# Kernel tuning notes

Hardware: AMD Instinct MI355X
Metric: run time of the kernel (lower is better)

The kernel has to match this reference:

```python
import jax, jax.numpy as jnp
import numpy as np

QMIN, QMAX = -128, 127  # get_quantized_range(8)


def setup_inputs() -> dict:
    key = jax.random.key(0)
    k1, k2, k3, k4 = jax.random.split(key, 4)
    N, IN, OUT = 8192, 4096, 4096
    x = jax.random.randint(k1, (N, IN), QMIN, QMAX + 1, dtype=jnp.int32).astype(jnp.int8)
    weight = jax.random.randint(k2, (OUT, IN), QMIN, QMAX + 1, dtype=jnp.int32).astype(jnp.int8)
    bias = jax.random.randint(k3, (OUT,), -1000, 1000, dtype=jnp.int32)
    weight_scale = jax.random.uniform(k4, (OUT,), dtype=jnp.float32, minval=1e-3, maxval=2e-2)
    return {
        "x": x,
        "weight": weight,
        "bias": bias,
        "weight_scale": weight_scale,
        "input_scale": 0.05,
        "output_scale": 0.1,
        "output_zero_point": -3,
    }


def reference(x, weight, bias, weight_scale, input_scale, output_scale, output_zero_point):
    # int8 GEMM accumulated in int32 (matches CPU path of the torch code)
    acc = jnp.matmul(x.astype(jnp.int32), weight.astype(jnp.int32).T) + bias[None, :]
    # fused per-channel dequant/requant epilogue
    scale = (input_scale * weight_scale / output_scale)[None, :]  # [1, OUT]
    out = acc.astype(jnp.float32) * scale + output_zero_point
    out = jnp.clip(jnp.round(out), QMIN, QMAX).astype(jnp.int8)
    return out
```

## Files before the change

### kernel.cpp

```cpp
#include <hip/hip_runtime.h>
#include <stdint.h>
#include <stddef.h>

typedef int v4i __attribute__((ext_vector_type(4)));

#define GLOAD16(gp, lp) __builtin_amdgcn_global_load_lds( \
    (const __attribute__((address_space(1))) void*)(gp),  \
    (__attribute__((address_space(3))) void*)(lp), 16, 0, 0)

#define PH_BAR()     __builtin_amdgcn_s_barrier()
#define WAIT_LGKM0() asm volatile("s_waitcnt lgkmcnt(0)" ::: "memory")
#define WAIT_VM(n)   asm volatile("s_waitcnt vmcnt(" #n ")" ::: "memory")
#define SCHED_FENCE() __builtin_amdgcn_sched_barrier(0)
#define PRIO1() __builtin_amdgcn_s_setprio(1)
#define PRIO0() __builtin_amdgcn_s_setprio(0)

static __device__ __forceinline__ int pack4(int a, int b, int c, int d) {
    return (a & 255) | ((b & 255) << 8) | ((c & 255) << 16) | (d << 24);
}

__global__ __launch_bounds__(256) void pack2_kernel(const int* __restrict__ srcA, v4i* __restrict__ dstA, int nA,
                                                    const int* __restrict__ srcB, v4i* __restrict__ dstB, int nB) {
    int i = blockIdx.x * blockDim.x + threadIdx.x;
    const int* src; v4i* dst;
    if (i < nA) { src = srcA; dst = dstA; }
    else { i -= nA; if (i >= nB) return; src = srcB; dst = dstB; }
    const v4i* s = reinterpret_cast<const v4i*>(src) + (size_t)i * 4;
    v4i v0 = s[0], v1 = s[1], v2 = s[2], v3 = s[3];
    v4i r;
    r.x = pack4(v0.x, v0.y, v0.z, v0.w);
    r.y = pack4(v1.x, v1.y, v1.z, v1.w);
    r.z = pack4(v2.x, v2.y, v2.z, v2.w);
    r.w = pack4(v3.x, v3.y, v3.z, v3.w);
    dst[i] = r;
}

__global__ __launch_bounds__(512, 2) void gemm_q8_8ph(
    const char* __restrict__ Apk, const char* __restrict__ Bpk,
    const int* __restrict__ bias, const float* __restrict__ wscale,
    const float* __restrict__ is_p, const float* __restrict__ os_p,
    const int* __restrict__ zp_p,
    int* __restrict__ out, int K, int Ncols)
{
    __shared__ char lds[131072];

    const int tid  = threadIdx.x;
    const int wid  = tid >> 6;
    const int lane = tid & 63;
    const int l7 = lane & 7, l3 = lane >> 3;
    const int lo16 = lane & 15, hi = lane >> 4;

    int swz;
    {
        const int nwg = gridDim.x;
        const int q = nwg >> 3, r = nwg & 7;
        const int xcd = blockIdx.x & 7;
        const int base = (xcd < r) ? xcd * (q + 1) : r * (q + 1) + (xcd - r) * q;
        swz = base + (blockIdx.x >> 3);
    }
    const int nbc  = Ncols >> 8;
    const int brow = swz / nbc, bcol = swz % nbc;

    const int wr = wid >> 2, wc = wid & 3;

    const char* Ab = Apk + (size_t)(brow * 256 + wid * 8 + l3) * K + ((l7 ^ l3) << 4);
    const char* Bb = Bpk + (size_t)(bcol * 256 + wid * 8 + l3) * K + ((l7 ^ l3) << 4);

    const int colsw0 = (hi << 4) ^ (l7 << 4);
    const int colsw1 = colsw0 ^ 64;
    const int aRow = ((wr << 7) + lo16) << 7;
    const int bRow = ((wc << 6) + lo16) << 7;

    v4i acc[8][4];
#pragma unroll
    for (int m = 0; m < 8; ++m)
#pragma unroll
        for (int n = 0; n < 4; ++n)
            acc[m][n] = (v4i){0, 0, 0, 0};

    v4i af[4][2], bf[2][2], bf2[2][2];

    auto stage = [&](const char* gb, int ldsOp, int bufo, int h, int t) {
        const char* g = gb + (size_t)(h * 128) * K + ((size_t)t << 7);
        char* l = lds + (ldsOp + bufo + (h << 14) + (wid << 10));
        GLOAD16(g, l);
        GLOAD16(g + (size_t)64 * K, l + 8192);
    };
    auto ldA = [&](int bufo, int mh) {
#pragma unroll
        for (int m = 0; m < 4; ++m) {
            const int base = bufo + aRow + (mh << 13) + (m << 11);
            af[m][0] = *(const v4i*)(lds + base + colsw0);
            af[m][1] = *(const v4i*)(lds + base + colsw1);
        }
    };
    auto ldB = [&](v4i (&bx)[2][2], int bufo, int n0) {
#pragma unroll
        for (int n = 0; n < 2; ++n) {
            const int base = 65536 + bufo + bRow + ((n0 + n) << 11);
            bx[n][0] = *(const v4i*)(lds + base + colsw0);
            bx[n][1] = *(const v4i*)(lds + base + colsw1);
        }
    };

#define MFMA_Q(mo, bfx, no) do {                                                  \
    _Pragma("unroll") for (int m_ = 0; m_ < 4; ++m_)                              \
    _Pragma("unroll") for (int n_ = 0; n_ < 2; ++n_)                              \
    _Pragma("unroll") for (int s_ = 0; s_ < 2; ++s_)                              \
        acc[(mo) + m_][(no) + n_] = __builtin_amdgcn_mfma_i32_16x16x64_i8(        \
            af[m_][s_], bfx[n_][s_], acc[(mo) + m_][(no) + n_], 0, 0, 0);         \
} while (0)

    stage(Ab, 0,     0,     0, 0);  stage(Ab, 0,     0,     1, 0);
    stage(Bb, 65536, 0,     0, 0);  stage(Bb, 65536, 0,     1, 0);
    stage(Bb, 65536, 32768, 0, 1);  stage(Bb, 65536, 32768, 1, 1);
    WAIT_VM(4);
    PH_BAR();
    ldB(bf, 0, 0);

    const int niter = K >> 8;
    for (int i = 0; i < niter - 1; ++i) {
        SCHED_FENCE();
        const int tO1 = 2 * i + 1, tE = 2 * i + 2, tO = 2 * i + 3;

        ldA(0, 0);
        stage(Ab, 0, 32768, 0, tO1);
        PH_BAR(); WAIT_LGKM0();
        PRIO1(); MFMA_Q(0, bf, 0); PRIO0();
        PH_BAR();
        ldB(bf2, 0, 2);
        stage(Ab, 0, 32768, 1, tO1);
        PH_BAR(); WAIT_LGKM0();
        PRIO1(); MFMA_Q(0, bf2, 2); PRIO0();
        PH_BAR();
        ldA(0, 1);
        stage(Bb, 65536, 0, 0, tE);
        PH_BAR(); WAIT_LGKM0();
        PRIO1(); MFMA_Q(4, bf, 0); PRIO0();
        WAIT_VM(6);
        PH_BAR();
        ldB(bf, 32768, 0);
        stage(Bb, 65536, 0, 1, tE);
        PH_BAR();
        PRIO1(); MFMA_Q(4, bf2, 2); PRIO0();
        WAIT_VM(4);
        PH_BAR();
        SCHED_FENCE();
        ldA(32768, 0);
        stage(Ab, 0, 0, 0, tE);
        PH_BAR(); WAIT_LGKM0();
        PRIO1(); MFMA_Q(0, bf, 0); PRIO0();
        PH_BAR();
        ldB(bf2, 32768, 2);
        stage(Ab, 0, 0, 1, tE);
        PH_BAR(); WAIT_LGKM0();
        PRIO1(); MFMA_Q(0, bf2, 2); PRIO0();
        PH_BAR();
        ldA(32768, 1);
        stage(Bb, 65536, 32768, 0, tO);
        PH_BAR(); WAIT_LGKM0();
        PRIO1(); MFMA_Q(4, bf, 0); PRIO0();
        WAIT_VM(6);
        PH_BAR();
        ldB(bf, 0, 0);
        stage(Bb, 65536, 32768, 1, tO);
        PH_BAR();
        PRIO1(); MFMA_Q(4, bf2, 2); PRIO0();
        WAIT_VM(4);
        PH_BAR();
    }

    {
        SCHED_FENCE();
        const int tL = 2 * niter - 1;
        ldA(0, 0);
        stage(Ab, 0, 32768, 0, tL);
        PH_BAR(); WAIT_LGKM0();
        PRIO1(); MFMA_Q(0, bf, 0); PRIO0();
        PH_BAR();
        ldB(bf2, 0, 2);
        stage(Ab, 0, 32768, 1, tL);
        PH_BAR(); WAIT_LGKM0();
        PRIO1(); MFMA_Q(0, bf2, 2); PRIO0();
        PH_BAR();
        ldA(0, 1);
        PH_BAR(); WAIT_LGKM0();
        PRIO1(); MFMA_Q(4, bf, 0); PRIO0();
        WAIT_VM(0);
        PH_BAR();
        ldB(bf, 32768, 0);
        PH_BAR();
        PRIO1(); MFMA_Q(4, bf2, 2); PRIO0();
        PH_BAR();
        ldA(32768, 0);
        PH_BAR(); WAIT_LGKM0();
        PRIO1(); MFMA_Q(0, bf, 0); PRIO0();
        PH_BAR();
        ldB(bf2, 32768, 2);
        PH_BAR(); WAIT_LGKM0();
        PRIO1(); MFMA_Q(0, bf2, 2); PRIO0();
        PH_BAR();
        ldA(32768, 1);
        PH_BAR(); WAIT_LGKM0();
        PRIO1(); MFMA_Q(4, bf, 0); PRIO0();
        PH_BAR();
        PRIO1(); MFMA_Q(4, bf2, 2); PRIO0();
    }
#undef MFMA_Q

    const float is = *is_p, os = *os_p;
    const float zp = (float)(*zp_p);
    const int colb = (bcol << 8) + (wc << 6) + lo16;
    float sc[4]; int bv[4];
#pragma unroll
    for (int n = 0; n < 4; ++n) {
        sc[n] = is * wscale[colb + (n << 4)] / os;
        bv[n] = bias[colb + (n << 4)];
    }
#pragma unroll
    for (int m = 0; m < 8; ++m) {
#pragma unroll
        for (int j = 0; j < 4; ++j) {
            const int row = (brow << 8) + (wr << 7) + (m << 4) + (hi << 2) + j;
            int* op = out + (size_t)row * Ncols + colb;
#pragma unroll
            for (int n = 0; n < 4; ++n) {
                float f = (float)(acc[m][n][j] + bv[n]) * sc[n] + zp;
                f = rintf(f);
                f = fminf(fmaxf(f, -128.f), 127.f);
                op[n << 4] = (int)f;
            }
        }
    }
}

template <bool PACKED>
__global__ __launch_bounds__(256) void gemm_q8(
    const void* __restrict__ Ain, const void* __restrict__ Bin,
    const int* __restrict__ bias, const float* __restrict__ wscale,
    const float* __restrict__ is_p, const float* __restrict__ os_p,
    const int* __restrict__ zp_p,
    int* __restrict__ out, int Nrows, int K, int Ncols)
{
    __shared__ char Al[128 * 64];
    __shared__ char Bl[128 * 64];

    const int tid  = threadIdx.x;
    const int wid  = tid >> 6;
    const int lane = tid & 63;

    const int nbc = Ncols / 128;
    int swz = blockIdx.x;
    if ((gridDim.x & 7) == 0) {
        const int cpx = gridDim.x >> 3;
        swz = (blockIdx.x & 7) * cpx + (blockIdx.x >> 3);
    }
    const int brow = swz / nbc;
    const int bcol = swz % nbc;
    const int wr = wid >> 1, wc = wid & 1;

    v4i acc[4][4];
#pragma unroll
    for (int m = 0; m < 4; ++m)
#pragma unroll
        for (int n = 0; n < 4; ++n)
            acc[m][n] = (v4i){0, 0, 0, 0};

    const char* Ag = nullptr;
    const char* Bg = nullptr;
    if (PACKED) {
        Ag = (const char*)Ain + (size_t)(brow * 128 + wid * 32 + (lane >> 2)) * K + (lane & 3) * 16;
        Bg = (const char*)Bin + (size_t)(bcol * 128 + wid * 32 + (lane >> 2)) * K + (lane & 3) * 16;
    }
    char* aldst = Al + wid * 2048;
    char* bldst = Bl + wid * 2048;

    const int lo16 = lane & 15, hi = lane >> 4;
    const int aoff0 = (wr * 64 + lo16) * 64 + hi * 16;
    const int boff0 = (wc * 64 + lo16) * 64 + hi * 16;

    for (int k0 = 0; k0 < K; k0 += 64) {
        if (PACKED) {
            GLOAD16(Ag + k0,          aldst);
            GLOAD16(Ag + 16 * K + k0, aldst + 1024);
            GLOAD16(Bg + k0,          bldst);
            GLOAD16(Bg + 16 * K + k0, bldst + 1024);
        } else {
            const int row = tid >> 1, half = tid & 1;
            const int* sA = (const int*)Ain + (size_t)(brow * 128 + row) * K + k0 + half * 32;
            const int* sB = (const int*)Bin + (size_t)(bcol * 128 + row) * K + k0 + half * 32;
            int pa[8], pb[8];
#pragma unroll
            for (int j = 0; j < 8; ++j) {
                v4i va = reinterpret_cast<const v4i*>(sA)[j];
                v4i vb = reinterpret_cast<const v4i*>(sB)[j];
                pa[j] = pack4(va.x, va.y, va.z, va.w);
                pb[j] = pack4(vb.x, vb.y, vb.z, vb.w);
            }
            v4i* da = (v4i*)&Al[row * 64 + half * 32];
            da[0] = (v4i){pa[0], pa[1], pa[2], pa[3]};
            da[1] = (v4i){pa[4], pa[5], pa[6], pa[7]};
            v4i* db = (v4i*)&Bl[row * 64 + half * 32];
            db[0] = (v4i){pb[0], pb[1], pb[2], pb[3]};
            db[1] = (v4i){pb[4], pb[5], pb[6], pb[7]};
        }
        __syncthreads();

        v4i af[4], bfr[4];
#pragma unroll
        for (int m = 0; m < 4; ++m)
            af[m] = *(const v4i*)&Al[aoff0 + m * 16 * 64];
#pragma unroll
        for (int n = 0; n < 4; ++n)
            bfr[n] = *(const v4i*)&Bl[boff0 + n * 16 * 64];
#pragma unroll
        for (int m = 0; m < 4; ++m)
#pragma unroll
            for (int n = 0; n < 4; ++n)
                acc[m][n] = __builtin_amdgcn_mfma_i32_16x16x64_i8(af[m], bfr[n], acc[m][n], 0, 0, 0);

        __syncthreads();
    }

    const float is = *is_p;
    const float os = *os_p;
    const float zp = (float)(*zp_p);
#pragma unroll
    for (int n = 0; n < 4; ++n) {
        const int col = bcol * 128 + wc * 64 + n * 16 + lo16;
        const float sc = is * wscale[col] / os;
        const int   bv = bias[col];
#pragma unroll
        for (int m = 0; m < 4; ++m) {
            const int row0 = brow * 128 + wr * 64 + m * 16 + hi * 4;
#pragma unroll
            for (int j = 0; j < 4; ++j) {
                float f = (float)(acc[m][n][j] + bv) * sc + zp;
                f = rintf(f);
                f = fminf(fmaxf(f, -128.f), 127.f);
                out[(size_t)(row0 + j) * Ncols + col] = (int)f;
            }
        }
    }
}

extern "C" void kernel_launch(void* const* d_in, const int* in_sizes, int n_in,
                              void* d_out, int out_size, void* d_ws, size_t ws_size,
                              hipStream_t stream) {
    const int*   x32    = (const int*)d_in[0];
    const int*   w32    = (const int*)d_in[1];
    const int*   bias   = (const int*)d_in[2];
    const float* wscale = (const float*)d_in[3];
    const float* isp    = (const float*)d_in[4];
    const float* osp    = (const float*)d_in[5];
    const int*   zpp    = (const int*)d_in[6];
    int* out = (int*)d_out;

    const int OUT = in_sizes[2];
    const int K   = in_sizes[1] / OUT;
    const int Nr  = in_sizes[0] / K;

    const size_t need = (size_t)Nr * K + (size_t)OUT * K;

    if (ws_size >= need) {
        char* xpk = (char*)d_ws;
        char* wpk = xpk + (size_t)Nr * K;
        const int nx16 = (Nr * K) / 16;
        const int nw16 = (OUT * K) / 16;
        pack2_kernel<<<(nx16 + nw16 + 255) / 256, 256, 0, stream>>>(
            x32, (v4i*)xpk, nx16, w32, (v4i*)wpk, nw16);
        if ((Nr & 255) == 0 && (OUT & 255) == 0 && (K & 511) == 0) {
            const int grid8 = (Nr / 256) * (OUT / 256);
            gemm_q8_8ph<<<grid8, 512, 0, stream>>>(xpk, wpk, bias, wscale, isp, osp, zpp,
                                                   out, K, OUT);
        } else {
            const int grid = (Nr / 128) * (OUT / 128);
            gemm_q8<true><<<grid, 256, 0, stream>>>(xpk, wpk, bias, wscale, isp, osp, zpp,
                                                    out, Nr, K, OUT);
        }
    } else {
        const int grid = (Nr / 128) * (OUT / 128);
        gemm_q8<false><<<grid, 256, 0, stream>>>(x32, w32, bias, wscale, isp, osp, zpp,
                                                 out, Nr, K, OUT);
    }
}
```

Measured before the change: 176.8 us.

## Switch main GEMM from 16x16x64 to 32x32x32 int8 MFMA tiles

Rewrites the warp-level tiling of the 8-phase int8 GEMM to use 32x32x32 MFMA instructions with 16-wide accumulators instead of 16x16x64. LDS fragment offsets, the swizzled column indices and the epilogue row/column mapping are recomputed for the 32x32 output layout. The aim is fewer MFMA issues and fewer LDS fragment reads per unit of work. In exchange, each fragment load now covers four K-slices, which may change LDS bank-conflict behaviour and register pressure.

```diff
diff --git a/kernel.cpp b/kernel.cpp
--- a/kernel.cpp
+++ b/kernel.cpp
@@ -2,7 +2,8 @@
 #include <stdint.h>
 #include <stddef.h>
 
-typedef int v4i __attribute__((ext_vector_type(4)));
+typedef int v4i  __attribute__((ext_vector_type(4)));
+typedef int v16i __attribute__((ext_vector_type(16)));
 
 #define GLOAD16(gp, lp) __builtin_amdgcn_global_load_lds( \
     (const __attribute__((address_space(1))) void*)(gp),  \
@@ -48,7 +49,7 @@
     const int wid  = tid >> 6;
     const int lane = tid & 63;
     const int l7 = lane & 7, l3 = lane >> 3;
-    const int lo16 = lane & 15, hi = lane >> 4;
+    const int l31 = lane & 31, hi5 = lane >> 5;
 
     int swz;
     {
@@ -66,19 +67,30 @@
     const char* Ab = Apk + (size_t)(brow * 256 + wid * 8 + l3) * K + ((l7 ^ l3) << 4);
     const char* Bb = Bpk + (size_t)(bcol * 256 + wid * 8 + l3) * K + ((l7 ^ l3) << 4);
 
-    const int colsw0 = (hi << 4) ^ (l7 << 4);
-    const int colsw1 = colsw0 ^ 64;
-    const int aRow = ((wr << 7) + lo16) << 7;
-    const int bRow = ((wc << 6) + lo16) << 7;
-
-    v4i acc[8][4];
-#pragma unroll
-    for (int m = 0; m < 8; ++m)
-#pragma unroll
-        for (int n = 0; n < 4; ++n)
-            acc[m][n] = (v4i){0, 0, 0, 0};
-
-    v4i af[4][2], bf[2][2], bf2[2][2];
+    int colw[4];
+#pragma unroll
+    for (int s = 0; s < 4; ++s) colw[s] = (((s << 1) + hi5) ^ l7) << 4;
+    int aOff[2][2];
+#pragma unroll
+    for (int mh = 0; mh < 2; ++mh)
+#pragma unroll
+        for (int m = 0; m < 2; ++m)
+            aOff[mh][m] = ((wr << 7) + (mh << 6) + (m << 5) + l31) << 7;
+    int bOff[2];
+#pragma unroll
+    for (int nj = 0; nj < 2; ++nj)
+        bOff[nj] = ((wc << 6) + (nj << 5) + l31) << 7;
+
+    v16i acc[4][2];
+#pragma unroll
+    for (int m = 0; m < 4; ++m)
+#pragma unroll
+        for (int n = 0; n < 2; ++n)
+#pragma unroll
+            for (int j = 0; j < 16; ++j)
+                acc[m][n][j] = 0;
+
+    v4i af[2][4], bf[4], bf2[4];
 
     auto stage = [&](const char* gb, int ldsOp, int bufo, int h, int t) {
         const char* g = gb + (size_t)(h * 128) * K + ((size_t)t << 7);
@@ -88,27 +100,22 @@
     };
     auto ldA = [&](int bufo, int mh) {
 #pragma unroll
-        for (int m = 0; m < 4; ++m) {
-            const int base = bufo + aRow + (mh << 13) + (m << 11);
-            af[m][0] = *(const v4i*)(lds + base + colsw0);
-            af[m][1] = *(const v4i*)(lds + base + colsw1);
-        }
+        for (int m = 0; m < 2; ++m)
+#pragma unroll
+            for (int s = 0; s < 4; ++s)
+                af[m][s] = *(const v4i*)(lds + bufo + aOff[mh][m] + colw[s]);
     };
-    auto ldB = [&](v4i (&bx)[2][2], int bufo, int n0) {
-#pragma unroll
-        for (int n = 0; n < 2; ++n) {
-            const int base = 65536 + bufo + bRow + ((n0 + n) << 11);
-            bx[n][0] = *(const v4i*)(lds + base + colsw0);
-            bx[n][1] = *(const v4i*)(lds + base + colsw1);
-        }
+    auto ldB = [&](v4i (&bx)[4], int bufo, int nj) {
+#pragma unroll
+        for (int s = 0; s < 4; ++s)
+            bx[s] = *(const v4i*)(lds + 65536 + bufo + bOff[nj] + colw[s]);
     };
 
-#define MFMA_Q(mo, bfx, no) do {                                                  \
-    _Pragma("unroll") for (int m_ = 0; m_ < 4; ++m_)                              \
-    _Pragma("unroll") for (int n_ = 0; n_ < 2; ++n_)                              \
-    _Pragma("unroll") for (int s_ = 0; s_ < 2; ++s_)                              \
-        acc[(mo) + m_][(no) + n_] = __builtin_amdgcn_mfma_i32_16x16x64_i8(        \
-            af[m_][s_], bfx[n_][s_], acc[(mo) + m_][(no) + n_], 0, 0, 0);         \
+#define MFMA_Q(mh, bfx, nIdx) do {                                                \
+    _Pragma("unroll") for (int m_ = 0; m_ < 2; ++m_)                              \
+    _Pragma("unroll") for (int s_ = 0; s_ < 4; ++s_)                              \
+        acc[((mh) << 1) + m_][nIdx] = __builtin_amdgcn_mfma_i32_32x32x32_i8(      \
+            af[m_][s_], bfx[s_], acc[((mh) << 1) + m_][nIdx], 0, 0, 0);           \
 } while (0)
 
     stage(Ab, 0,     0,     0, 0);  stage(Ab, 0,     0,     1, 0);
@@ -128,21 +135,21 @@
         PH_BAR(); WAIT_LGKM0();
         PRIO1(); MFMA_Q(0, bf, 0); PRIO0();
         PH_BAR();
-        ldB(bf2, 0, 2);
+        ldB(bf2, 0, 1);
         stage(Ab, 0, 32768, 1, tO1);
         PH_BAR(); WAIT_LGKM0();
-        PRIO1(); MFMA_Q(0, bf2, 2); PRIO0();
+        PRIO1(); MFMA_Q(0, bf2, 1); PRIO0();
         PH_BAR();
         ldA(0, 1);
         stage(Bb, 65536, 0, 0, tE);
         PH_BAR(); WAIT_LGKM0();
-        PRIO1(); MFMA_Q(4, bf, 0); PRIO0();
+        PRIO1(); MFMA_Q(1, bf, 0); PRIO0();
         WAIT_VM(6);
         PH_BAR();
         ldB(bf, 32768, 0);
         stage(Bb, 65536, 0, 1, tE);
         PH_BAR();
-        PRIO1(); MFMA_Q(4, bf2, 2); PRIO0();
+        PRIO1(); MFMA_Q(1, bf2, 1); PRIO0();
         WAIT_VM(4);
         PH_BAR();
         SCHED_FENCE();
@@ -151,21 +158,21 @@
         PH_BAR(); WAIT_LGKM0();
         PRIO1(); MFMA_Q(0, bf, 0); PRIO0();
         PH_BAR();
-        ldB(bf2, 32768, 2);
+        ldB(bf2, 32768, 1);
         stage(Ab, 0, 0, 1, tE);
         PH_BAR(); WAIT_LGKM0();
-        PRIO1(); MFMA_Q(0, bf2, 2); PRIO0();
+        PRIO1(); MFMA_Q(0, bf2, 1); PRIO0();
         PH_BAR();
         ldA(32768, 1);
         stage(Bb, 65536, 32768, 0, tO);
         PH_BAR(); WAIT_LGKM0();
-        PRIO1(); MFMA_Q(4, bf, 0); PRIO0();
+        PRIO1(); MFMA_Q(1, bf, 0); PRIO0();
         WAIT_VM(6);
         PH_BAR();
         ldB(bf, 0, 0);
         stage(Bb, 65536, 32768, 1, tO);
         PH_BAR();
-        PRIO1(); MFMA_Q(4, bf2, 2); PRIO0();
+        PRIO1(); MFMA_Q(1, bf2, 1); PRIO0();
         WAIT_VM(4);
         PH_BAR();
     }
@@ -178,57 +185,61 @@
         PH_BAR(); WAIT_LGKM0();
         PRIO1(); MFMA_Q(0, bf, 0); PRIO0();
         PH_BAR();
-        ldB(bf2, 0, 2);
+        ldB(bf2, 0, 1);
         stage(Ab, 0, 32768, 1, tL);
         PH_BAR(); WAIT_LGKM0();
-        PRIO1(); MFMA_Q(0, bf2, 2); PRIO0();
+        PRIO1(); MFMA_Q(0, bf2, 1); PRIO0();
         PH_BAR();
         ldA(0, 1);
         PH_BAR(); WAIT_LGKM0();
-        PRIO1(); MFMA_Q(4, bf, 0); PRIO0();
+        PRIO1(); MFMA_Q(1, bf, 0); PRIO0();
         WAIT_VM(0);
         PH_BAR();
         ldB(bf, 32768, 0);
         PH_BAR();
-        PRIO1(); MFMA_Q(4, bf2, 2); PRIO0();
+        PRIO1(); MFMA_Q(1, bf2, 1); PRIO0();
         PH_BAR();
         ldA(32768, 0);
         PH_BAR(); WAIT_LGKM0();
         PRIO1(); MFMA_Q(0, bf, 0); PRIO0();
         PH_BAR();
-        ldB(bf2, 32768, 2);
-        PH_BAR(); WAIT_LGKM0();
-        PRIO1(); MFMA_Q(0, bf2, 2); PRIO0();
+        ldB(bf2, 32768, 1);
+        PH_BAR(); WAIT_LGKM0();
+        PRIO1(); MFMA_Q(0, bf2, 1); PRIO0();
         PH_BAR();
         ldA(32768, 1);
         PH_BAR(); WAIT_LGKM0();
-        PRIO1(); MFMA_Q(4, bf, 0); PRIO0();
-        PH_BAR();
-        PRIO1(); MFMA_Q(4, bf2, 2); PRIO0();
+        PRIO1(); MFMA_Q(1, bf, 0); PRIO0();
+        PH_BAR();
+        PRIO1(); MFMA_Q(1, bf2, 1); PRIO0();
     }
 #undef MFMA_Q
 
     const float is = *is_p, os = *os_p;
     const float zp = (float)(*zp_p);
-    const int colb = (bcol << 8) + (wc << 6) + lo16;
-    float sc[4]; int bv[4];
-#pragma unroll
-    for (int n = 0; n < 4; ++n) {
-        sc[n] = is * wscale[colb + (n << 4)] / os;
-        bv[n] = bias[colb + (n << 4)];
-    }
-#pragma unroll
-    for (int m = 0; m < 8; ++m) {
-#pragma unroll
-        for (int j = 0; j < 4; ++j) {
-            const int row = (brow << 8) + (wr << 7) + (m << 4) + (hi << 2) + j;
-            int* op = out + (size_t)row * Ncols + colb;
-#pragma unroll
-            for (int n = 0; n < 4; ++n) {
-                float f = (float)(acc[m][n][j] + bv[n]) * sc[n] + zp;
-                f = rintf(f);
-                f = fminf(fmaxf(f, -128.f), 127.f);
-                op[n << 4] = (int)f;
+    const int colb = (bcol << 8) + (wc << 6) + l31;
+    float sc[2]; int bv[2];
+#pragma unroll
+    for (int nj = 0; nj < 2; ++nj) {
+        sc[nj] = is * wscale[colb + (nj << 5)] / os;
+        bv[nj] = bias[colb + (nj << 5)];
+    }
+#pragma unroll
+    for (int mf = 0; mf < 4; ++mf) {
+        const int rowbase = (brow << 8) + (wr << 7) + (mf << 5) + (hi5 << 2);
+#pragma unroll
+        for (int rg = 0; rg < 4; ++rg) {
+#pragma unroll
+            for (int j = 0; j < 4; ++j) {
+                const int row = rowbase + (rg << 3) + j;
+                int* op = out + (size_t)row * Ncols + colb;
+#pragma unroll
+                for (int nj = 0; nj < 2; ++nj) {
+                    float f = (float)(acc[mf][nj][(rg << 2) + j] + bv[nj]) * sc[nj] + zp;
+                    f = rintf(f);
+                    f = fminf(fmaxf(f, -128.f), 127.f);
+                    op[nj << 5] = (int)f;
+                }
             }
         }
     }
@@ -306,10 +317,10 @@
         }
         __syncthreads();
 
-        v4i af[4], bfr[4];
+        v4i afr[4], bfr[4];
 #pragma unroll
         for (int m = 0; m < 4; ++m)
-            af[m] = *(const v4i*)&Al[aoff0 + m * 16 * 64];
+            afr[m] = *(const v4i*)&Al[aoff0 + m * 16 * 64];
 #pragma unroll
         for (int n = 0; n < 4; ++n)
             bfr[n] = *(const v4i*)&Bl[boff0 + n * 16 * 64];
@@ -317,7 +328,7 @@
         for (int m = 0; m < 4; ++m)
 #pragma unroll
             for (int n = 0; n < 4; ++n)
-                acc[m][n] = __builtin_amdgcn_mfma_i32_16x16x64_i8(af[m], bfr[n], acc[m][n], 0, 0, 0);
+                acc[m][n] = __builtin_amdgcn_mfma_i32_16x16x64_i8(afr[m], bfr[n], acc[m][n], 0, 0, 0);
 
         __syncthreads();
     }
```

Result: slower. 202.9 us (+14.8%).

## Double-buffer A/B fragment registers and remove explicit LDS waits in GEMM pipeline

Applied to the files above, without the earlier changes.

Restructures the int8 MFMA main loop so that A and B fragments are held in two register sets (afA/afB, bfA/bf2). LDS reads for the next quarter are issued before the current quarter's MFMAs run, which lets the explicit lgkmcnt(0) waits be dropped. The prologue is reordered to stage A's second tile instead of B's, and barriers per quarter are reduced, with sched fences enforcing order. This aims to hide LDS latency behind MFMA work and cut barrier stalls, at the cost of more VGPRs and relying on compiler-inserted waits for correctness.

```diff
diff --git a/kernel.cpp b/kernel.cpp
--- a/kernel.cpp
+++ b/kernel.cpp
@@ -9,7 +9,6 @@
     (__attribute__((address_space(3))) void*)(lp), 16, 0, 0)
 
 #define PH_BAR()     __builtin_amdgcn_s_barrier()
-#define WAIT_LGKM0() asm volatile("s_waitcnt lgkmcnt(0)" ::: "memory")
 #define WAIT_VM(n)   asm volatile("s_waitcnt vmcnt(" #n ")" ::: "memory")
 #define SCHED_FENCE() __builtin_amdgcn_sched_barrier(0)
 #define PRIO1() __builtin_amdgcn_s_setprio(1)
@@ -78,7 +77,7 @@
         for (int n = 0; n < 4; ++n)
             acc[m][n] = (v4i){0, 0, 0, 0};
 
-    v4i af[4][2], bf[2][2], bf2[2][2];
+    v4i afA[4][2], afB[4][2], bfA[2][2], bf2[2][2];
 
     auto stage = [&](const char* gb, int ldsOp, int bufo, int h, int t) {
         const char* g = gb + (size_t)(h * 128) * K + ((size_t)t << 7);
@@ -86,127 +85,132 @@
         GLOAD16(g, l);
         GLOAD16(g + (size_t)64 * K, l + 8192);
     };
-    auto ldA = [&](int bufo, int mh) {
+    auto ldAf = [&](v4i (&dst)[4][2], int bufo, int mh) {
 #pragma unroll
         for (int m = 0; m < 4; ++m) {
             const int base = bufo + aRow + (mh << 13) + (m << 11);
-            af[m][0] = *(const v4i*)(lds + base + colsw0);
-            af[m][1] = *(const v4i*)(lds + base + colsw1);
+            dst[m][0] = *(const v4i*)(lds + base + colsw0);
+            dst[m][1] = *(const v4i*)(lds + base + colsw1);
         }
     };
-    auto ldB = [&](v4i (&bx)[2][2], int bufo, int n0) {
+    auto ldBf = [&](v4i (&dst)[2][2], int bufo, int n0) {
 #pragma unroll
         for (int n = 0; n < 2; ++n) {
             const int base = 65536 + bufo + bRow + ((n0 + n) << 11);
-            bx[n][0] = *(const v4i*)(lds + base + colsw0);
-            bx[n][1] = *(const v4i*)(lds + base + colsw1);
+            dst[n][0] = *(const v4i*)(lds + base + colsw0);
+            dst[n][1] = *(const v4i*)(lds + base + colsw1);
         }
     };
 
-#define MFMA_Q(mo, bfx, no) do {                                                  \
+#define MQ(afX, bfX, mo, no) do {                                                 \
     _Pragma("unroll") for (int m_ = 0; m_ < 4; ++m_)                              \
     _Pragma("unroll") for (int n_ = 0; n_ < 2; ++n_)                              \
     _Pragma("unroll") for (int s_ = 0; s_ < 2; ++s_)                              \
         acc[(mo) + m_][(no) + n_] = __builtin_amdgcn_mfma_i32_16x16x64_i8(        \
-            af[m_][s_], bfx[n_][s_], acc[(mo) + m_][(no) + n_], 0, 0, 0);         \
+            afX[m_][s_], bfX[n_][s_], acc[(mo) + m_][(no) + n_], 0, 0, 0);        \
 } while (0)
 
     stage(Ab, 0,     0,     0, 0);  stage(Ab, 0,     0,     1, 0);
     stage(Bb, 65536, 0,     0, 0);  stage(Bb, 65536, 0,     1, 0);
-    stage(Bb, 65536, 32768, 0, 1);  stage(Bb, 65536, 32768, 1, 1);
+    stage(Ab, 0,     32768, 0, 1);  stage(Ab, 0,     32768, 1, 1);
     WAIT_VM(4);
     PH_BAR();
-    ldB(bf, 0, 0);
+    SCHED_FENCE();
+    ldAf(afA, 0, 0);
+    ldBf(bfA, 0, 0);
 
     const int niter = K >> 8;
     for (int i = 0; i < niter - 1; ++i) {
-        SCHED_FENCE();
-        const int tO1 = 2 * i + 1, tE = 2 * i + 2, tO = 2 * i + 3;
-
-        ldA(0, 0);
-        stage(Ab, 0, 32768, 0, tO1);
-        PH_BAR(); WAIT_LGKM0();
-        PRIO1(); MFMA_Q(0, bf, 0); PRIO0();
-        PH_BAR();
-        ldB(bf2, 0, 2);
-        stage(Ab, 0, 32768, 1, tO1);
-        PH_BAR(); WAIT_LGKM0();
-        PRIO1(); MFMA_Q(0, bf2, 2); PRIO0();
-        PH_BAR();
-        ldA(0, 1);
-        stage(Bb, 65536, 0, 0, tE);
-        PH_BAR(); WAIT_LGKM0();
-        PRIO1(); MFMA_Q(4, bf, 0); PRIO0();
-        WAIT_VM(6);
-        PH_BAR();
-        ldB(bf, 32768, 0);
-        stage(Bb, 65536, 0, 1, tE);
-        PH_BAR();
-        PRIO1(); MFMA_Q(4, bf2, 2); PRIO0();
-        WAIT_VM(4);
-        PH_BAR();
-        SCHED_FENCE();
-        ldA(32768, 0);
-        stage(Ab, 0, 0, 0, tE);
-        PH_BAR(); WAIT_LGKM0();
-        PRIO1(); MFMA_Q(0, bf, 0); PRIO0();
-        PH_BAR();
-        ldB(bf2, 32768, 2);
-        stage(Ab, 0, 0, 1, tE);
-        PH_BAR(); WAIT_LGKM0();
-        PRIO1(); MFMA_Q(0, bf2, 2); PRIO0();
-        PH_BAR();
-        ldA(32768, 1);
+        const int tO = 2 * i + 1, tE2 = 2 * i + 2, tO2 = 2 * i + 3;
+
+        SCHED_FENCE();
+        ldBf(bf2, 0, 2);
+        ldAf(afB, 0, 1);
         stage(Bb, 65536, 32768, 0, tO);
-        PH_BAR(); WAIT_LGKM0();
-        PRIO1(); MFMA_Q(4, bf, 0); PRIO0();
-        WAIT_VM(6);
-        PH_BAR();
-        ldB(bf, 0, 0);
+        SCHED_FENCE();
+        PRIO1(); MQ(afA, bfA, 0, 0); PRIO0();
+        PH_BAR();
+        SCHED_FENCE();
         stage(Bb, 65536, 32768, 1, tO);
-        PH_BAR();
-        PRIO1(); MFMA_Q(4, bf2, 2); PRIO0();
-        WAIT_VM(4);
+        SCHED_FENCE();
+        PRIO1(); MQ(afA, bf2, 0, 2); PRIO0();
+        PH_BAR();
+        SCHED_FENCE();
+        stage(Ab, 0, 0, 0, tE2);
+        SCHED_FENCE();
+        PRIO1(); MQ(afB, bfA, 4, 0); PRIO0();
+        WAIT_VM(2);
+        PH_BAR();
+        SCHED_FENCE();
+        ldAf(afA, 32768, 0);
+        ldBf(bfA, 32768, 0);
+        stage(Ab, 0, 0, 1, tE2);
+        SCHED_FENCE();
+        PRIO1(); MQ(afB, bf2, 4, 2); PRIO0();
+        PH_BAR();
+        SCHED_FENCE();
+        ldBf(bf2, 32768, 2);
+        ldAf(afB, 32768, 1);
+        stage(Bb, 65536, 0, 0, tE2);
+        SCHED_FENCE();
+        PRIO1(); MQ(afA, bfA, 0, 0); PRIO0();
+        PH_BAR();
+        SCHED_FENCE();
+        stage(Bb, 65536, 0, 1, tE2);
+        SCHED_FENCE();
+        PRIO1(); MQ(afA, bf2, 0, 2); PRIO0();
+        PH_BAR();
+        SCHED_FENCE();
+        stage(Ab, 0, 32768, 0, tO2);
+        SCHED_FENCE();
+        PRIO1(); MQ(afB, bfA, 4, 0); PRIO0();
+        WAIT_VM(2);
+        PH_BAR();
+        SCHED_FENCE();
+        ldAf(afA, 0, 0);
+        ldBf(bfA, 0, 0);
+        stage(Ab, 0, 32768, 1, tO2);
+        SCHED_FENCE();
+        PRIO1(); MQ(afB, bf2, 4, 2); PRIO0();
         PH_BAR();
     }
 
     {
-        SCHED_FENCE();
-        const int tL = 2 * niter - 1;
-        ldA(0, 0);
-        stage(Ab, 0, 32768, 0, tL);
-        PH_BAR(); WAIT_LGKM0();
-        PRIO1(); MFMA_Q(0, bf, 0); PRIO0();
-        PH_BAR();
-        ldB(bf2, 0, 2);
-        stage(Ab, 0, 32768, 1, tL);
-        PH_BAR(); WAIT_LGKM0();
-        PRIO1(); MFMA_Q(0, bf2, 2); PRIO0();
-        PH_BAR();
-        ldA(0, 1);
-        PH_BAR(); WAIT_LGKM0();
-        PRIO1(); MFMA_Q(4, bf, 0); PRIO0();
+        const int tO = 2 * niter - 1;
+        SCHED_FENCE();
+        ldBf(bf2, 0, 2);
+        ldAf(afB, 0, 1);
+        stage(Bb, 65536, 32768, 0, tO);
+        SCHED_FENCE();
+        PRIO1(); MQ(afA, bfA, 0, 0); PRIO0();
+        PH_BAR();
+        SCHED_FENCE();
+        stage(Bb, 65536, 32768, 1, tO);
+        SCHED_FENCE();
+        PRIO1(); MQ(afA, bf2, 0, 2); PRIO0();
+        PH_BAR();
+        PRIO1(); MQ(afB, bfA, 4, 0); PRIO0();
         WAIT_VM(0);
         PH_BAR();
-        ldB(bf, 32768, 0);
-        PH_BAR();
-        PRIO1(); MFMA_Q(4, bf2, 2); PRIO0();
-        PH_BAR();
-        ldA(32768, 0);
-        PH_BAR(); WAIT_LGKM0();
-        PRIO1(); MFMA_Q(0, bf, 0); PRIO0();
-        PH_BAR();
-        ldB(bf2, 32768, 2);
-        PH_BAR(); WAIT_LGKM0();
-        PRIO1(); MFMA_Q(0, bf2, 2); PRIO0();
-        PH_BAR();
-        ldA(32768, 1);
-        PH_BAR(); WAIT_LGKM0();
-        PRIO1(); MFMA_Q(4, bf, 0); PRIO0();
-        PH_BAR();
-        PRIO1(); MFMA_Q(4, bf2, 2); PRIO0();
-    }
-#undef MFMA_Q
+        SCHED_FENCE();
+        ldAf(afA, 32768, 0);
+        ldBf(bfA, 32768, 0);
+        SCHED_FENCE();
+        PRIO1(); MQ(afB, bf2, 4, 2); PRIO0();
+        PH_BAR();
+        SCHED_FENCE();
+        ldBf(bf2, 32768, 2);
+        ldAf(afB, 32768, 1);
+        SCHED_FENCE();
+        PRIO1(); MQ(afA, bfA, 0, 0); PRIO0();
+        PH_BAR();
+        PRIO1(); MQ(afA, bf2, 0, 2); PRIO0();
+        PH_BAR();
+        PRIO1(); MQ(afB, bfA, 4, 0); PRIO0();
+        PH_BAR();
+        PRIO1(); MQ(afB, bf2, 4, 2); PRIO0();
+    }
+#undef MQ
 
     const float is = *is_p, os = *os_p;
     const float zp = (float)(*zp_p);
@@ -306,10 +310,10 @@
         }
         __syncthreads();
 
-        v4i af[4], bfr[4];
+        v4i afr[4], bfr[4];
 #pragma unroll
         for (int m = 0; m < 4; ++m)
-            af[m] = *(const v4i*)&Al[aoff0 + m * 16 * 64];
+            afr[m] = *(const v4i*)&Al[aoff0 + m * 16 * 64];
 #pragma unroll
         for (int n = 0; n < 4; ++n)
             bfr[n] = *(const v4i*)&Bl[boff0 + n * 16 * 64];
@@ -317,7 +321,7 @@
         for (int m = 0; m < 4; ++m)
 #pragma unroll
             for (int n = 0; n < 4; ++n)
-                acc[m][n] = __builtin_amdgcn_mfma_i32_16x16x64_i8(af[m], bfr[n], acc[m][n], 0, 0, 0);
+                acc[m][n] = __builtin_amdgcn_mfma_i32_16x16x64_i8(afr[m], bfr[n], acc[m][n], 0, 0, 0);
 
         __syncthreads();
     }
```

New measurement: 292.3 us. +65.4%, slower.
